# Kernel tuning notes

Measured on AMD Instinct MI355X. Metric: run time of the kernel, lower is better.

## Reference

```python
import jax, jax.numpy as jnp
import numpy as np

FRAMES, RANK = 128, 5          # rank=5 implied by create_adj6 non_adj index lists (max index 4)
N = FRAMES * RANK              # 640 nodes
B, NFEAT, NHID, NCLASS = 128, 256, 8, 16
ALPHA = 0.2                    # LeakyReLU negative slope
MASK_VAL = -9e15               # hard mask value from the torch code


def create_adj6(frames, rank):
    """Block-diagonal (with holes) + chain adjacency, exactly as in the torch source."""
    adj = np.zeros((frames * rank, frames * rank), dtype=np.float32)
    non_adj_x = [0, 0, 1, 2, 3, 3, 4, 4]
    non_adj_y = [3, 4, 4, 3, 0, 2, 0, 1]
    for i in range(frames):
        adj[rank * i:rank * (i + 1), rank * i:rank * (i + 1)] = 1
        for j in range(len(non_adj_x)):
            adj[rank * i + non_adj_x[j], rank * i + non_adj_y[j]] = 0
        for j in range(rank):
            if i > 0:
                adj[rank * i + j, rank * (i - 1) + j] = 1
            if i < frames - 1:
                adj[rank * i + j, rank * (i + 1) + j] = 1
    return adj


def _xavier(key, shape):
    fan_in, fan_out = shape[0], shape[1]
    std = np.sqrt(2.0) * np.sqrt(2.0 / (fan_in + fan_out))  # gain=sqrt(2) xavier_normal
    return std * jax.random.normal(key, shape, dtype=jnp.float32)


def setup_inputs() -> dict:
    key = jax.random.key(0)
    ks = jax.random.split(key, 7)
    x = jax.random.normal(ks[0], (B, N, NFEAT), dtype=jnp.float32)
    W1 = _xavier(ks[1], (NFEAT, NHID))
    a11 = _xavier(ks[2], (NHID, 1))
    a12 = _xavier(ks[3], (NHID, 1))
    W2 = _xavier(ks[4], (NHID, NCLASS))  # nhid*nheads=8 -> nclass=16
    a21 = _xavier(ks[5], (NCLASS, 1))
    a22 = _xavier(ks[6], (NCLASS, 1))
    adj = jnp.asarray(create_adj6(FRAMES, RANK) > 0)  # bool [N, N]
    return dict(x=x, W1=W1, a11=a11, a12=a12, W2=W2, a21=a21, a22=a22, adj=adj)


def gat_layer(xi, adj, W, a1, a2):
    # xi: [N, F_in]
    h = xi @ W                              # [N, F_out]
    f1 = h @ a1                             # [N, 1]
    f2 = h @ a2                             # [N, 1]
    e = jax.nn.leaky_relu(f1 + f2.T, negative_slope=ALPHA)  # [N, N]
    scores = jnp.where(adj, e, jnp.float32(MASK_VAL))        # hard additive-style mask
    att = jax.nn.softmax(scores, axis=-1)   # dropout disabled (eval mode)
    return att @ h                          # [N, F_out]


def reference(x, W1, a11, a12, W2, a21, a22, adj):
    def single(xi):
        h1 = gat_layer(xi, adj, W1, a11, a12)          # concat=False -> no elu inside layer
        h2 = jax.nn.elu(gat_layer(h1, adj, W2, a21, a22))
        return jax.nn.log_softmax(h2, axis=1)          # [N, NCLASS]
    return jax.vmap(single)(x)                          # [B, N, NCLASS]
```

## Files before the change

### kernel.cpp

```cpp
#include <hip/hip_runtime.h>

#define B_ 128
#define N_ 640
#define NFEAT 256
#define NHID 8
#define NCLASS 16
#define RANK 5
#define FRAMES 128
#define ALPHA 0.2f
#define PACKMASK 30236135u

#define QSPLIT 8
#define TFRAMES (FRAMES / QSPLIT)
#define TCOUNT (TFRAMES * RANK)
#define BLOCKT 256
#define MAXSTAGE 100
#define H1S 9
#define H2S 17

#define OFF_F1S (MAXSTAGE * H1S)
#define OFF_F2S (OFF_F1S + MAXSTAGE)
#define OFF_HPART (OFF_F2S + MAXSTAGE)
#define OFF_G1S (MAXSTAGE * H2S)
#define OFF_G2S (OFF_G1S + MAXSTAGE)
#define SMEMF (OFF_HPART + MAXSTAGE * H1S)

typedef float f2 __attribute__((ext_vector_type(2)));

__device__ __forceinline__ float lrelu(float v) { return v >= 0.0f ? v : ALPHA * v; }

__global__ void __launch_bounds__(BLOCKT, 4) k_fused(
    const float* __restrict__ x, const float* __restrict__ W1,
    const float* __restrict__ a11, const float* __restrict__ a12,
    const float* __restrict__ W2, const float* __restrict__ a21, const float* __restrict__ a22,
    float* __restrict__ out)
{
    __shared__ float smem[SMEMF];
    float* h1s = smem;
    float* f1s = smem + OFF_F1S;
    float* f2s = smem + OFF_F2S;
    float* h2s = smem;
    float* g1s = smem + OFF_G1S;
    float* g2s = smem + OFF_G2S;

    const int bid = blockIdx.x;
    const int bq  = (bid & 7) * 128 + (bid >> 3);
    const int b   = bq >> 3;
    const int q   = bq & 7;

    const int tf_lo  = q * TFRAMES;
    const int l1f_lo = max(tf_lo - 1, 0);
    const int l1f_hi = min(tf_lo + TFRAMES, FRAMES - 1);
    const int stf_lo = max(tf_lo - 2, 0);
    const int stf_hi = min(tf_lo + TFRAMES + 1, FRAMES - 1);
    const int stage_lo  = stf_lo * RANK;
    const int stage_cnt = (stf_hi - stf_lo + 1) * RANK;
    const int l1_lo  = l1f_lo * RANK;
    const int l1_cnt = (l1f_hi - l1f_lo + 1) * RANK;
    const int t_lo   = tf_lo * RANK;

    const int tid  = threadIdx.x;
    const int half = __builtin_amdgcn_readfirstlane(tid >> 7);
    const int r    = tid & 127;
    const int rowc = (r < stage_cnt) ? r : (stage_cnt - 1);

    f2 h01 = {0.f, 0.f}, h23 = {0.f, 0.f}, h45 = {0.f, 0.f}, h67 = {0.f, 0.f};
    {
        const float* xr = x + ((size_t)b * N_ + stage_lo + rowc) * NFEAT + (half << 7);
        const float* wb = W1 + (half << 10);

#pragma unroll
        for (int c = 0; c < 32; ++c) {
            const float4 xv = *reinterpret_cast<const float4*>(xr + 4 * c);
            const f2* wr = reinterpret_cast<const f2*>(wb + (c << 5));
            f2 xs;
            xs.x = xv.x; xs.y = xv.x;
            h01 = __builtin_elementwise_fma(xs, wr[0], h01);
            h23 = __builtin_elementwise_fma(xs, wr[1], h23);
            h45 = __builtin_elementwise_fma(xs, wr[2], h45);
            h67 = __builtin_elementwise_fma(xs, wr[3], h67);
            xs.x = xv.y; xs.y = xv.y;
            h01 = __builtin_elementwise_fma(xs, wr[4], h01);
            h23 = __builtin_elementwise_fma(xs, wr[5], h23);
            h45 = __builtin_elementwise_fma(xs, wr[6], h45);
            h67 = __builtin_elementwise_fma(xs, wr[7], h67);
            xs.x = xv.z; xs.y = xv.z;
            h01 = __builtin_elementwise_fma(xs, wr[8], h01);
            h23 = __builtin_elementwise_fma(xs, wr[9], h23);
            h45 = __builtin_elementwise_fma(xs, wr[10], h45);
            h67 = __builtin_elementwise_fma(xs, wr[11], h67);
            xs.x = xv.w; xs.y = xv.w;
            h01 = __builtin_elementwise_fma(xs, wr[12], h01);
            h23 = __builtin_elementwise_fma(xs, wr[13], h23);
            h45 = __builtin_elementwise_fma(xs, wr[14], h45);
            h67 = __builtin_elementwise_fma(xs, wr[15], h67);
        }
    }
    if (half && r < stage_cnt) {
        float* hp = smem + OFF_HPART + r * H1S;
        hp[0] = h01.x; hp[1] = h01.y; hp[2] = h23.x; hp[3] = h23.y;
        hp[4] = h45.x; hp[5] = h45.y; hp[6] = h67.x; hp[7] = h67.y;
    }
    __syncthreads();

    if (tid < stage_cnt) {
        const float* hp = smem + OFF_HPART + tid * H1S;
        float hv[NHID];
        hv[0] = h01.x + hp[0]; hv[1] = h01.y + hp[1];
        hv[2] = h23.x + hp[2]; hv[3] = h23.y + hp[3];
        hv[4] = h45.x + hp[4]; hv[5] = h45.y + hp[5];
        hv[6] = h67.x + hp[6]; hv[7] = h67.y + hp[7];
        float s1 = 0.0f, s2 = 0.0f;
#pragma unroll
        for (int k = 0; k < NHID; ++k) {
            s1 = fmaf(hv[k], a11[k], s1);
            s2 = fmaf(hv[k], a12[k], s2);
            h1s[tid * H1S + k] = hv[k];
        }
        f1s[tid] = s1;
        f2s[tid] = s2;
    }
    __syncthreads();

    float h2[NCLASS];
    float s1g = 0.0f, s2g = 0.0f;
    const bool actL1 = (tid < l1_cnt);
    if (actL1) {
        const int u  = l1_lo + tid;
        const int fr = u / RANK;
        const int ru = u - fr * RANK;
        const unsigned rm = (PACKMASK >> (5 * ru)) & 31u;
        const int loc      = u - stage_lo;
        const int base_loc = fr * RANK - stage_lo;
        const bool hp = (fr > 0), hn = (fr < FRAMES - 1);
        const float fu = f1s[loc];

        float m = -1e30f;
        if (hp) m = fmaxf(m, lrelu(fu + f2s[loc - RANK]));
#pragma unroll
        for (int rv = 0; rv < RANK; ++rv)
            if (rm & (1u << rv)) m = fmaxf(m, lrelu(fu + f2s[base_loc + rv]));
        if (hn) m = fmaxf(m, lrelu(fu + f2s[loc + RANK]));

        float s = 0.0f;
        float o1[NHID];
#pragma unroll
        for (int k = 0; k < NHID; ++k) o1[k] = 0.0f;

        auto acc1 = [&](int vloc) {
            float w = __expf(lrelu(fu + f2s[vloc]) - m);
            s += w;
#pragma unroll
            for (int k = 0; k < NHID; ++k) o1[k] = fmaf(w, h1s[vloc * H1S + k], o1[k]);
        };
        if (hp) acc1(loc - RANK);
#pragma unroll
        for (int rv = 0; rv < RANK; ++rv)
            if (rm & (1u << rv)) acc1(base_loc + rv);
        if (hn) acc1(loc + RANK);

        const float inv = 1.0f / s;
#pragma unroll
        for (int k = 0; k < NHID; ++k) o1[k] *= inv;

#pragma unroll
        for (int c = 0; c < NCLASS; ++c) {
            float t = 0.0f;
#pragma unroll
            for (int k = 0; k < NHID; ++k) t = fmaf(o1[k], W2[k * NCLASS + c], t);
            h2[c] = t;
            s1g = fmaf(t, a21[c], s1g);
            s2g = fmaf(t, a22[c], s2g);
        }
    }
    __syncthreads();

    if (actL1) {
        const int loc = l1_lo + tid - stage_lo;
#pragma unroll
        for (int c = 0; c < NCLASS; ++c) h2s[loc * H2S + c] = h2[c];
        g1s[loc] = s1g;
        g2s[loc] = s2g;
    }
    __syncthreads();

    if (tid < TCOUNT) {
        const int u  = t_lo + tid;
        const int fr = u / RANK;
        const int ru = u - fr * RANK;
        const unsigned rm = (PACKMASK >> (5 * ru)) & 31u;
        const int loc      = u - stage_lo;
        const int base_loc = fr * RANK - stage_lo;
        const bool hp = (fr > 0), hn = (fr < FRAMES - 1);
        const float gu = g1s[loc];

        float m = -1e30f;
        if (hp) m = fmaxf(m, lrelu(gu + g2s[loc - RANK]));
#pragma unroll
        for (int rv = 0; rv < RANK; ++rv)
            if (rm & (1u << rv)) m = fmaxf(m, lrelu(gu + g2s[base_loc + rv]));
        if (hn) m = fmaxf(m, lrelu(gu + g2s[loc + RANK]));

        float s = 0.0f;
        float o2[NCLASS];
#pragma unroll
        for (int c = 0; c < NCLASS; ++c) o2[c] = 0.0f;

        auto acc2 = [&](int vloc) {
            float w = __expf(lrelu(gu + g2s[vloc]) - m);
            s += w;
#pragma unroll
            for (int c = 0; c < NCLASS; ++c) o2[c] = fmaf(w, h2s[vloc * H2S + c], o2[c]);
        };
        if (hp) acc2(loc - RANK);
#pragma unroll
        for (int rv = 0; rv < RANK; ++rv)
            if (rm & (1u << rv)) acc2(base_loc + rv);
        if (hn) acc2(loc + RANK);

        const float inv = 1.0f / s;
#pragma unroll
        for (int c = 0; c < NCLASS; ++c) o2[c] *= inv;

#pragma unroll
        for (int c = 0; c < NCLASS; ++c) o2[c] = (o2[c] > 0.0f) ? o2[c] : __expf(o2[c]) - 1.0f;

        float mm = o2[0];
#pragma unroll
        for (int c = 1; c < NCLASS; ++c) mm = fmaxf(mm, o2[c]);
        float ss = 0.0f;
#pragma unroll
        for (int c = 0; c < NCLASS; ++c) ss += __expf(o2[c] - mm);
        const float ls = mm + __logf(ss);

        float* op = out + ((size_t)b * N_ + u) * NCLASS;
#pragma unroll
        for (int c = 0; c < NCLASS; c += 4)
            *reinterpret_cast<float4*>(op + c) =
                make_float4(o2[c] - ls, o2[c + 1] - ls, o2[c + 2] - ls, o2[c + 3] - ls);
    }
}

extern "C" void kernel_launch(void* const* d_in, const int* in_sizes, int n_in,
                              void* d_out, int out_size, void* d_ws, size_t ws_size,
                              hipStream_t stream)
{
    const float* x   = (const float*)d_in[0];
    const float* W1  = (const float*)d_in[1];
    const float* a11 = (const float*)d_in[2];
    const float* a12 = (const float*)d_in[3];
    const float* W2  = (const float*)d_in[4];
    const float* a21 = (const float*)d_in[5];
    const float* a22 = (const float*)d_in[6];
    float* outp = (float*)d_out;

    k_fused<<<B_ * QSPLIT, BLOCKT, 0, stream>>>(x, W1, a11, a12, W2, a21, a22, outp);
}
```

Before: 28.96 us.

## Split fused kernel into streaming x@W1 GEMM and separate attention kernel

```diff
diff --git a/kernel.cpp b/kernel.cpp
--- a/kernel.cpp
+++ b/kernel.cpp
@@ -1,4 +1,5 @@
 #include <hip/hip_runtime.h>
+#include <stdint.h>
 
 #define B_ 128
 #define N_ 640
@@ -10,69 +11,39 @@
 #define ALPHA 0.2f
 #define PACKMASK 30236135u
 
-#define QSPLIT 8
-#define TFRAMES (FRAMES / QSPLIT)
-#define TCOUNT (TFRAMES * RANK)
-#define BLOCKT 256
-#define MAXSTAGE 100
-#define H1S 9
-#define H2S 17
-
-#define OFF_F1S (MAXSTAGE * H1S)
-#define OFF_F2S (OFF_F1S + MAXSTAGE)
-#define OFF_HPART (OFF_F2S + MAXSTAGE)
-#define OFF_G1S (MAXSTAGE * H2S)
-#define OFF_G2S (OFF_G1S + MAXSTAGE)
-#define SMEMF (OFF_HPART + MAXSTAGE * H1S)
-
+typedef float f4 __attribute__((ext_vector_type(4)));
 typedef float f2 __attribute__((ext_vector_type(2)));
 
-__device__ __forceinline__ float lrelu(float v) { return v >= 0.0f ? v : ALPHA * v; }
-
-__global__ void __launch_bounds__(BLOCKT, 4) k_fused(
+#define GR_BLOCK 64
+#define GR_GRID (B_ * N_ / GR_BLOCK)
+
+__global__ void __launch_bounds__(GR_BLOCK) k_gemm(
     const float* __restrict__ x, const float* __restrict__ W1,
-    const float* __restrict__ a11, const float* __restrict__ a12,
-    const float* __restrict__ W2, const float* __restrict__ a21, const float* __restrict__ a22,
-    float* __restrict__ out)
+    float* __restrict__ h1ws)
 {
-    __shared__ float smem[SMEMF];
-    float* h1s = smem;
-    float* f1s = smem + OFF_F1S;
-    float* f2s = smem + OFF_F2S;
-    float* h2s = smem;
-    float* g1s = smem + OFF_G1S;
-    float* g2s = smem + OFF_G2S;
-
-    const int bid = blockIdx.x;
-    const int bq  = (bid & 7) * 128 + (bid >> 3);
-    const int b   = bq >> 3;
-    const int q   = bq & 7;
-
-    const int tf_lo  = q * TFRAMES;
-    const int l1f_lo = max(tf_lo - 1, 0);
-    const int l1f_hi = min(tf_lo + TFRAMES, FRAMES - 1);
-    const int stf_lo = max(tf_lo - 2, 0);
-    const int stf_hi = min(tf_lo + TFRAMES + 1, FRAMES - 1);
-    const int stage_lo  = stf_lo * RANK;
-    const int stage_cnt = (stf_hi - stf_lo + 1) * RANK;
-    const int l1_lo  = l1f_lo * RANK;
-    const int l1_cnt = (l1f_hi - l1f_lo + 1) * RANK;
-    const int t_lo   = tf_lo * RANK;
-
-    const int tid  = threadIdx.x;
-    const int half = __builtin_amdgcn_readfirstlane(tid >> 7);
-    const int r    = tid & 127;
-    const int rowc = (r < stage_cnt) ? r : (stage_cnt - 1);
+    const int row = blockIdx.x * GR_BLOCK + threadIdx.x;
+    const f4* xr = reinterpret_cast<const f4*>(x + (size_t)row * NFEAT);
 
     f2 h01 = {0.f, 0.f}, h23 = {0.f, 0.f}, h45 = {0.f, 0.f}, h67 = {0.f, 0.f};
-    {
-        const float* xr = x + ((size_t)b * N_ + stage_lo + rowc) * NFEAT + (half << 7);
-        const float* wb = W1 + (half << 10);
-
-#pragma unroll
-        for (int c = 0; c < 32; ++c) {
-            const float4 xv = *reinterpret_cast<const float4*>(xr + 4 * c);
-            const f2* wr = reinterpret_cast<const f2*>(wb + (c << 5));
+
+    f4 xa[16], xb[16];
+#pragma unroll
+    for (int i = 0; i < 16; ++i) xa[i] = __builtin_nontemporal_load(xr + i);
+
+#pragma unroll
+    for (int t = 0; t < 4; ++t) {
+        const f4* cur = (t & 1) ? xb : xa;
+        f4*       nxt = (t & 1) ? xa : xb;
+        if (t < 3) {
+#pragma unroll
+            for (int i = 0; i < 16; ++i)
+                nxt[i] = __builtin_nontemporal_load(xr + (t + 1) * 16 + i);
+        }
+        const float* wbase = W1 + t * 64 * NHID;
+#pragma unroll
+        for (int i = 0; i < 16; ++i) {
+            const f4 xv = cur[i];
+            const f2* wr = reinterpret_cast<const f2*>(wbase + i * 4 * NHID);
             f2 xs;
             xs.x = xv.x; xs.y = xv.x;
             h01 = __builtin_elementwise_fma(xs, wr[0], h01);
@@ -96,20 +67,68 @@
             h67 = __builtin_elementwise_fma(xs, wr[15], h67);
         }
     }
-    if (half && r < stage_cnt) {
-        float* hp = smem + OFF_HPART + r * H1S;
-        hp[0] = h01.x; hp[1] = h01.y; hp[2] = h23.x; hp[3] = h23.y;
-        hp[4] = h45.x; hp[5] = h45.y; hp[6] = h67.x; hp[7] = h67.y;
-    }
-    __syncthreads();
+
+    float* hp = h1ws + (size_t)row * NHID;
+    f4 o0, o1v;
+    o0.x = h01.x; o0.y = h01.y; o0.z = h23.x; o0.w = h23.y;
+    o1v.x = h45.x; o1v.y = h45.y; o1v.z = h67.x; o1v.w = h67.y;
+    *reinterpret_cast<f4*>(hp)     = o0;
+    *reinterpret_cast<f4*>(hp + 4) = o1v;
+}
+
+#define QSPLIT 8
+#define TFRAMES (FRAMES / QSPLIT)
+#define TCOUNT (TFRAMES * RANK)
+#define BLOCKB 128
+#define MAXSTAGE 100
+#define H1S 9
+#define H2S 17
+
+#define OFF_F1S (MAXSTAGE * H1S)
+#define OFF_F2S (OFF_F1S + MAXSTAGE)
+#define OFF_G1S (MAXSTAGE * H2S)
+#define OFF_G2S (OFF_G1S + MAXSTAGE)
+#define SMEMF (OFF_G2S + MAXSTAGE)
+
+__device__ __forceinline__ float lrelu(float v) { return v >= 0.0f ? v : ALPHA * v; }
+
+__global__ void __launch_bounds__(BLOCKB, 8) k_attn(
+    const float* __restrict__ h1ws,
+    const float* __restrict__ a11, const float* __restrict__ a12,
+    const float* __restrict__ W2, const float* __restrict__ a21, const float* __restrict__ a22,
+    float* __restrict__ out)
+{
+    __shared__ float smem[SMEMF];
+    float* h1s = smem;
+    float* f1s = smem + OFF_F1S;
+    float* f2s = smem + OFF_F2S;
+    float* h2s = smem;
+    float* g1s = smem + OFF_G1S;
+    float* g2s = smem + OFF_G2S;
+
+    const int bid = blockIdx.x;
+    const int bq  = (bid & 7) * 128 + (bid >> 3);
+    const int b   = bq >> 3;
+    const int q   = bq & 7;
+
+    const int tf_lo  = q * TFRAMES;
+    const int l1f_lo = max(tf_lo - 1, 0);
+    const int l1f_hi = min(tf_lo + TFRAMES, FRAMES - 1);
+    const int stf_lo = max(tf_lo - 2, 0);
+    const int stf_hi = min(tf_lo + TFRAMES + 1, FRAMES - 1);
+    const int stage_lo  = stf_lo * RANK;
+    const int stage_cnt = (stf_hi - stf_lo + 1) * RANK;
+    const int l1_lo  = l1f_lo * RANK;
+    const int l1_cnt = (l1f_hi - l1f_lo + 1) * RANK;
+    const int t_lo   = tf_lo * RANK;
+
+    const int tid = threadIdx.x;
 
     if (tid < stage_cnt) {
-        const float* hp = smem + OFF_HPART + tid * H1S;
-        float hv[NHID];
-        hv[0] = h01.x + hp[0]; hv[1] = h01.y + hp[1];
-        hv[2] = h23.x + hp[2]; hv[3] = h23.y + hp[3];
-        hv[4] = h45.x + hp[4]; hv[5] = h45.y + hp[5];
-        hv[6] = h67.x + hp[6]; hv[7] = h67.y + hp[7];
+        const float* hp = h1ws + ((size_t)b * N_ + stage_lo + tid) * NHID;
+        const float4 p = *reinterpret_cast<const float4*>(hp);
+        const float4 q4 = *reinterpret_cast<const float4*>(hp + 4);
+        float hv[NHID] = {p.x, p.y, p.z, p.w, q4.x, q4.y, q4.z, q4.w};
         float s1 = 0.0f, s2 = 0.0f;
 #pragma unroll
         for (int k = 0; k < NHID; ++k) {
@@ -252,7 +271,9 @@
     const float* W2  = (const float*)d_in[4];
     const float* a21 = (const float*)d_in[5];
     const float* a22 = (const float*)d_in[6];
-    float* outp = (float*)d_out;
-
-    k_fused<<<B_ * QSPLIT, BLOCKT, 0, stream>>>(x, W1, a11, a12, W2, a21, a22, outp);
+    float* outp  = (float*)d_out;
+    float* h1ws  = (float*)d_ws;
+
+    k_gemm<<<GR_GRID, GR_BLOCK, 0, stream>>>(x, W1, h1ws);
+    k_attn<<<B_ * QSPLIT, BLOCKB, 0, stream>>>(h1ws, a11, a12, W2, a21, a22, outp);
 }
```

New measurement: 54.98 us. 1.9x slower.
